# Optimization experiments

Hardware: AMD Instinct MI355X
Metric: run time of the kernel (lower is better)

## Reference

```python
import jax, jax.numpy as jnp
import numpy as np

D_MODEL = 768
EXPAND = 2
D_INNER = EXPAND * D_MODEL  # 1536
D_STATE = 16
D_CONV = 4
DT_RANK = D_MODEL // 16  # 48
N_LAYER = 3
BATCH, SEQLEN = 2, 1024
EPS = 1e-5


def setup_inputs() -> dict:
    key = jax.random.key(0)
    ks = jax.random.split(key, 8)
    s = 0.02
    hidden_states = jax.random.normal(ks[0], (BATCH, SEQLEN, D_MODEL), jnp.float32)
    norm_w = jnp.ones((N_LAYER, D_MODEL), jnp.float32)
    in_proj_w = s * jax.random.normal(ks[1], (N_LAYER, 2 * D_INNER, D_MODEL), jnp.float32)
    conv_w = s * jax.random.normal(ks[2], (N_LAYER, D_INNER, D_CONV), jnp.float32)
    conv_b = jnp.zeros((N_LAYER, D_INNER), jnp.float32)
    x_proj_w = s * jax.random.normal(ks[3], (N_LAYER, DT_RANK + 2 * D_STATE, D_INNER), jnp.float32)
    dt_proj_w = s * jax.random.normal(ks[4], (N_LAYER, D_INNER, DT_RANK), jnp.float32)
    dt_proj_b = jnp.full((N_LAYER, D_INNER), -4.6, jnp.float32)  # softplus ~ 0.01
    # S4D-real init: A_log = log(1..d_state), tiled over channels
    A_log = jnp.tile(jnp.log(jnp.arange(1, D_STATE + 1, dtype=jnp.float32))[None, None, :], (N_LAYER, D_INNER, 1))
    D_skip = jnp.ones((N_LAYER, D_INNER), jnp.float32)
    out_proj_w = s * jax.random.normal(ks[5], (N_LAYER, D_MODEL, D_INNER), jnp.float32)
    norm_f_w = jnp.ones((D_MODEL,), jnp.float32)
    return dict(hidden_states=hidden_states, norm_w=norm_w, in_proj_w=in_proj_w,
                conv_w=conv_w, conv_b=conv_b, x_proj_w=x_proj_w, dt_proj_w=dt_proj_w,
                dt_proj_b=dt_proj_b, A_log=A_log, D_skip=D_skip, out_proj_w=out_proj_w,
                norm_f_w=norm_f_w)


def _rmsnorm(x, w):
    return x * jax.lax.rsqrt(jnp.mean(x * x, axis=-1, keepdims=True) + EPS) * w


def _causal_conv1d(x, w, b):
    # x: [B, L, D]; w: [D, K] depthwise; left-pad for causality
    xt = jnp.transpose(x, (0, 2, 1))  # [B, D, L]
    y = jax.lax.conv_general_dilated(xt, w[:, None, :], window_strides=(1,),
                                     padding=[(D_CONV - 1, 0)], feature_group_count=D_INNER)
    return jnp.transpose(y, (0, 2, 1)) + b


def _selective_scan(u, delta, A, Bc, Cc, Dp):
    # u, delta: [B, L, D]; A: [D, N]; Bc, Cc: [B, L, N]
    def step(h, inp):
        dt, bt, ct, ut = inp  # [B,D], [B,N], [B,N], [B,D]
        h = jnp.exp(dt[..., None] * A) * h + (dt * ut)[..., None] * bt[:, None, :]
        y = jnp.einsum('bdn,bn->bd', h, ct)
        return h, y
    h0 = jnp.zeros((u.shape[0], u.shape[2], A.shape[1]), u.dtype)
    xs = (jnp.swapaxes(delta, 0, 1), jnp.swapaxes(Bc, 0, 1), jnp.swapaxes(Cc, 0, 1), jnp.swapaxes(u, 0, 1))
    _, ys = jax.lax.scan(step, h0, xs)  # ys: [L, B, D]
    return jnp.swapaxes(ys, 0, 1) + u * Dp


def _mixer(h, in_w, cw, cb, xw, dtw, dtb, A_log, Dp, ow):
    xz = jnp.einsum('bld,ed->ble', h, in_w)  # [B, L, 2*D_INNER]
    x, z = xz[..., :D_INNER], xz[..., D_INNER:]
    x = jax.nn.silu(_causal_conv1d(x, cw, cb))
    x_dbl = jnp.einsum('bld,ed->ble', x, xw)
    dt = x_dbl[..., :DT_RANK]
    Bc = x_dbl[..., DT_RANK:DT_RANK + D_STATE]
    Cc = x_dbl[..., DT_RANK + D_STATE:]
    delta = jax.nn.softplus(jnp.einsum('blr,dr->bld', dt, dtw) + dtb)
    A = -jnp.exp(A_log)
    y = _selective_scan(x, delta, A, Bc, Cc, Dp)
    y = y * jax.nn.silu(z)
    return jnp.einsum('bld,ed->ble', y, ow)


def reference(hidden_states, norm_w, in_proj_w, conv_w, conv_b, x_proj_w, dt_proj_w,
              dt_proj_b, A_log, D_skip, out_proj_w, norm_f_w):
    hidden = hidden_states
    residual = None
    for i in range(N_LAYER):
        residual = hidden if residual is None else hidden + residual  # fused add
        hidden = _rmsnorm(residual, norm_w[i])
        hidden = _mixer(hidden, in_proj_w[i], conv_w[i], conv_b[i], x_proj_w[i],
                        dt_proj_w[i], dt_proj_b[i], A_log[i], D_skip[i], out_proj_w[i])
    # final fused add + RMSNorm (prenorm=False)
    return _rmsnorm(hidden + residual, norm_f_w)
```

## Files before the change

### kernel.cpp

```cpp
#include <hip/hip_runtime.h>
#include <math.h>

#define D_MODEL 768
#define D_INNER 1536
#define D_STATE 16
#define D_CONV 4
#define DT_RANK 48
#define N_LAYER 3
#define BATCH 2
#define SEQLEN 1024
#define NROWS (BATCH * SEQLEN)
#define XDBL_W (DT_RANK + 2 * D_STATE)
#define EPS 1e-5f

#define SCHUNKS 64
#define SCLEN 16
#define SDN 16
#define KSPLIT 4
#define KSLICE (D_INNER / KSPLIT)

typedef short bf16x8 __attribute__((ext_vector_type(8)));
typedef float f32x4 __attribute__((ext_vector_type(4)));

__device__ __forceinline__ ushort f2bf(float x) {
    union { float f; uint u; } v; v.f = x;
    uint r = v.u + 0x7fff + ((v.u >> 16) & 1);
    return (ushort)(r >> 16);
}

__device__ __forceinline__ void gload_lds16(const void* g, void* l) {
    __builtin_amdgcn_global_load_lds(
        (const __attribute__((address_space(1))) unsigned int*)g,
        (__attribute__((address_space(3))) unsigned int*)l, 16, 0, 0);
}

__global__ __launch_bounds__(256) void cvt_bf16_kernel(
    const float* __restrict__ s, ushort* __restrict__ d, int n4)
{
    int i = blockIdx.x * 256 + threadIdx.x;
    if (i >= n4) return;
    float4 v = ((const float4*)s)[i];
    ushort4 o;
    o.x = f2bf(v.x); o.y = f2bf(v.y); o.z = f2bf(v.z); o.w = f2bf(v.w);
    ((ushort4*)d)[i] = o;
}

__global__ __launch_bounds__(256) void add_rmsnorm_kernel(
    const float* __restrict__ x, const float* __restrict__ res_in,
    const float* __restrict__ w, float* __restrict__ res_out,
    float* __restrict__ normed_f32, ushort* __restrict__ normed_bf)
{
    int row = blockIdx.x;
    int tid = threadIdx.x;
    const float* xr = x + row * D_MODEL;
    float v[3];
    float ss = 0.f;
#pragma unroll
    for (int i = 0; i < 3; i++) {
        int c = tid + i * 256;
        float t = xr[c];
        if (res_in) t += res_in[row * D_MODEL + c];
        v[i] = t;
        ss += t * t;
    }
    for (int off = 32; off; off >>= 1) ss += __shfl_xor(ss, off, 64);
    __shared__ float red[4];
    if ((tid & 63) == 0) red[tid >> 6] = ss;
    __syncthreads();
    float tot = red[0] + red[1] + red[2] + red[3];
    float scale = rsqrtf(tot * (1.f / D_MODEL) + EPS);
#pragma unroll
    for (int i = 0; i < 3; i++) {
        int c = tid + i * 256;
        if (res_out) res_out[row * D_MODEL + c] = v[i];
        float o = v[i] * scale * w[c];
        if (normed_f32) normed_f32[row * D_MODEL + c] = o;
        if (normed_bf)  normed_bf[row * D_MODEL + c] = f2bf(o);
    }
}

template <int BM, int BN>
__global__ __launch_bounds__(256) void gemm_mfma_kernel(
    const ushort* __restrict__ A, const ushort* __restrict__ W,
    float* __restrict__ C, int M, int N, int K)
{
    constexpr int TM = BM / 32;
    constexpr int TN = BN / 32;
    __shared__ __attribute__((aligned(16))) ushort As[BM * 64];
    __shared__ __attribute__((aligned(16))) ushort Ws[BN * 64];
    const int t = threadIdx.x;
    const int lane = t & 63, w = t >> 6;
    const int ln15 = lane & 15, q = lane >> 4;
    const int row0 = blockIdx.y * BM, col0 = blockIdx.x * BN;
    const int wm0 = (w & 1) * (BM / 2), wn0 = (w >> 1) * (BN / 2);

    f32x4 acc[TM][TN];
#pragma unroll
    for (int i = 0; i < TM; i++)
#pragma unroll
        for (int j = 0; j < TN; j++) acc[i][j] = (f32x4){0.f, 0.f, 0.f, 0.f};

    for (int k0 = 0; k0 < K; k0 += 64) {
        __syncthreads();
#pragma unroll
        for (int i = 0; i < BM / 32; i++) {
            int p = (i * 4 + w) * 64 + lane;
            int r = p >> 3, s = p & 7;
            int g = s ^ (r & 7);
            gload_lds16(A + (size_t)(row0 + r) * K + k0 + g * 8, &As[p * 8]);
        }
#pragma unroll
        for (int i = 0; i < BN / 32; i++) {
            int p = (i * 4 + w) * 64 + lane;
            int r = p >> 3, s = p & 7;
            int g = s ^ (r & 7);
            gload_lds16(W + (size_t)(col0 + r) * K + k0 + g * 8, &Ws[p * 8]);
        }
        __syncthreads();
#pragma unroll
        for (int ks = 0; ks < 2; ks++) {
            bf16x8 af[TM], wf[TN];
#pragma unroll
            for (int im = 0; im < TM; im++) {
                int m = wm0 + im * 16 + ln15;
                int slot = (ks * 4 + q) ^ (m & 7);
                af[im] = *(const bf16x8*)&As[m * 64 + slot * 8];
            }
#pragma unroll
            for (int jn = 0; jn < TN; jn++) {
                int n = wn0 + jn * 16 + ln15;
                int slot = (ks * 4 + q) ^ (n & 7);
                wf[jn] = *(const bf16x8*)&Ws[n * 64 + slot * 8];
            }
#pragma unroll
            for (int im = 0; im < TM; im++)
#pragma unroll
                for (int jn = 0; jn < TN; jn++)
                    acc[im][jn] = __builtin_amdgcn_mfma_f32_16x16x32_bf16(
                        af[im], wf[jn], acc[im][jn], 0, 0, 0);
        }
    }
#pragma unroll
    for (int im = 0; im < TM; im++) {
#pragma unroll
        for (int jn = 0; jn < TN; jn++) {
            int rr = row0 + wm0 + im * 16 + q * 4;
            int cc = col0 + wn0 + jn * 16 + ln15;
            float* cp = C + (size_t)rr * N + cc;
#pragma unroll
            for (int r = 0; r < 4; r++) cp[(size_t)r * N] = acc[im][jn][r];
        }
    }
}

template <int EPI>
__global__ __launch_bounds__(256) void gemm_kernel(
    const float* __restrict__ A, int lda,
    const float* __restrict__ W,
    const float* __restrict__ bias,
    float* __restrict__ C, int ldc,
    int M, int N, int K)
{
    __shared__ float As[16][64];
    __shared__ float Wsh[16][64];
    int tid = threadIdx.x;
    int row0 = blockIdx.y * 64;
    int col0 = blockIdx.x * 64;
    int lm = tid >> 2;
    int lk = (tid & 3) * 4;
    int ty = tid >> 4, tx = tid & 15;
    float acc[4][4] = {};
    const float* Arow = A + (size_t)(row0 + lm) * lda + lk;
    const float* Wrow = W + (size_t)(col0 + lm) * K + lk;
    bool wvalid = (col0 + lm) < N;

    for (int k0 = 0; k0 < K; k0 += 16) {
        float4 av = *(const float4*)(Arow + k0);
        float4 wv = wvalid ? *(const float4*)(Wrow + k0) : make_float4(0.f, 0.f, 0.f, 0.f);
        __syncthreads();
        As[lk + 0][lm] = av.x; As[lk + 1][lm] = av.y;
        As[lk + 2][lm] = av.z; As[lk + 3][lm] = av.w;
        Wsh[lk + 0][lm] = wv.x; Wsh[lk + 1][lm] = wv.y;
        Wsh[lk + 2][lm] = wv.z; Wsh[lk + 3][lm] = wv.w;
        __syncthreads();
#pragma unroll
        for (int k = 0; k < 16; k++) {
            float4 a = *(const float4*)&As[k][ty * 4];
            float4 b = *(const float4*)&Wsh[k][tx * 4];
            float ar[4] = {a.x, a.y, a.z, a.w};
            float br[4] = {b.x, b.y, b.z, b.w};
#pragma unroll
            for (int i = 0; i < 4; i++)
#pragma unroll
                for (int j = 0; j < 4; j++) acc[i][j] += ar[i] * br[j];
        }
    }
#pragma unroll
    for (int i = 0; i < 4; i++) {
        int r = row0 + ty * 4 + i;
#pragma unroll
        for (int j = 0; j < 4; j++) {
            int c = col0 + tx * 4 + j;
            if (c < N) {
                float v = acc[i][j];
                if (EPI == 1) {
                    v += bias[c];
                    v = (v > 20.f) ? v : log1pf(__expf(v));
                }
                C[(size_t)r * ldc + c] = v;
            }
        }
    }
}

__global__ __launch_bounds__(256) void gemm_xpart_kernel(
    const float* __restrict__ A, const float* __restrict__ W,
    float* __restrict__ Cp)
{
    __shared__ float As[16][64];
    __shared__ float Wsh[16][64];
    int tid = threadIdx.x;
    int row0 = blockIdx.y * 64;
    int col0 = blockIdx.x * 64;
    int kz = blockIdx.z * KSLICE;
    int lm = tid >> 2;
    int lk = (tid & 3) * 4;
    int ty = tid >> 4, tx = tid & 15;
    float acc[4][4] = {};
    const float* Arow = A + (size_t)(row0 + lm) * D_INNER + kz + lk;
    const float* Wrow = W + (size_t)(col0 + lm) * D_INNER + kz + lk;
    bool wvalid = (col0 + lm) < XDBL_W;

    for (int k0 = 0; k0 < KSLICE; k0 += 16) {
        float4 av = *(const float4*)(Arow + k0);
        float4 wv = wvalid ? *(const float4*)(Wrow + k0) : make_float4(0.f, 0.f, 0.f, 0.f);
        __syncthreads();
        As[lk + 0][lm] = av.x; As[lk + 1][lm] = av.y;
        As[lk + 2][lm] = av.z; As[lk + 3][lm] = av.w;
        Wsh[lk + 0][lm] = wv.x; Wsh[lk + 1][lm] = wv.y;
        Wsh[lk + 2][lm] = wv.z; Wsh[lk + 3][lm] = wv.w;
        __syncthreads();
#pragma unroll
        for (int k = 0; k < 16; k++) {
            float4 a = *(const float4*)&As[k][ty * 4];
            float4 b = *(const float4*)&Wsh[k][tx * 4];
            float ar[4] = {a.x, a.y, a.z, a.w};
            float br[4] = {b.x, b.y, b.z, b.w};
#pragma unroll
            for (int i = 0; i < 4; i++)
#pragma unroll
                for (int j = 0; j < 4; j++) acc[i][j] += ar[i] * br[j];
        }
    }
    float* Co = Cp + (size_t)blockIdx.z * NROWS * XDBL_W;
#pragma unroll
    for (int i = 0; i < 4; i++) {
        int r = row0 + ty * 4 + i;
#pragma unroll
        for (int j = 0; j < 4; j++) {
            int c = col0 + tx * 4 + j;
            if (c < XDBL_W) Co[(size_t)r * XDBL_W + c] = acc[i][j];
        }
    }
}

__global__ __launch_bounds__(256) void xreduce_kernel(
    const float* __restrict__ Cp, float* __restrict__ xdbl)
{
    int i = blockIdx.x * 256 + threadIdx.x;
    const int S4 = NROWS * XDBL_W / 4;
    if (i >= S4) return;
    const float4* p = (const float4*)Cp;
    float4 a = p[i], b = p[i + S4], c = p[i + 2 * S4], d = p[i + 3 * S4];
    float4 o;
    o.x = a.x + b.x + c.x + d.x;
    o.y = a.y + b.y + c.y + d.y;
    o.z = a.z + b.z + c.z + d.z;
    o.w = a.w + b.w + c.w + d.w;
    ((float4*)xdbl)[i] = o;
}

__global__ __launch_bounds__(256) void conv_silu_kernel(
    const float* __restrict__ xz, const float* __restrict__ cw,
    const float* __restrict__ cb, float* __restrict__ out)
{
    int idx = blockIdx.x * 256 + threadIdx.x;
    int d = idx % D_INNER;
    int bl = idx / D_INNER;
    int l = bl % SEQLEN;
    float s = cb[d];
    const float* xp = xz + (size_t)bl * (2 * D_INNER) + d;
#pragma unroll
    for (int k = 0; k < D_CONV; k++) {
        int ls = l - (D_CONV - 1) + k;
        if (ls >= 0) s += cw[d * D_CONV + k] * xp[(k - (D_CONV - 1)) * (2 * D_INNER)];
    }
    out[(size_t)bl * D_INNER + d] = s / (1.f + __expf(-s));
}

__global__ __launch_bounds__(1024) void scan2_kernel(
    const float* __restrict__ u, const float* __restrict__ delta,
    const float* __restrict__ A_log, const float* __restrict__ xdbl,
    const float* __restrict__ Dskip, const float* __restrict__ xz,
    ushort* __restrict__ ybf)
{
    __shared__ float PL[16][SDN * 17];
    __shared__ float HL[16][SDN * 17];
    const int t = threadIdx.x;
    const int lane = t & 63;
    const int w = t >> 6;
    const int dsub = lane & 15;
    const int csub = lane >> 4;
    const int c = w * 4 + csub;
    const int b = blockIdx.x / (D_INNER / SDN);
    const int d = (blockIdx.x % (D_INNER / SDN)) * SDN + dsub;

    float a2[D_STATE];
#pragma unroll
    for (int n = 0; n < D_STATE; n++)
        a2[n] = -__expf(A_log[d * D_STATE + n]) * 1.44269504f;

    const size_t base = (size_t)b * SEQLEN * D_INNER + d;
    const float* dtp = delta + base;
    const float* up  = u + base;
    const float* xrow = xdbl + (size_t)b * SEQLEN * XDBL_W;
    const int l0 = c * SCLEN;

    float h[D_STATE], P[D_STATE];
#pragma unroll
    for (int n = 0; n < D_STATE; n++) { h[n] = 0.f; P[n] = 1.f; }

    for (int i = 0; i < SCLEN; i++) {
        const int l = l0 + i;
        float dt = dtp[(size_t)l * D_INNER];
        float uu = up[(size_t)l * D_INNER];
        const float4* Bv = (const float4*)(xrow + (size_t)l * XDBL_W + DT_RANK);
        float4 q0 = Bv[0], q1 = Bv[1], q2 = Bv[2], q3 = Bv[3];
        float Bf[D_STATE] = {q0.x,q0.y,q0.z,q0.w, q1.x,q1.y,q1.z,q1.w,
                             q2.x,q2.y,q2.z,q2.w, q3.x,q3.y,q3.z,q3.w};
        float dtu = dt * uu;
#pragma unroll
        for (int n = 0; n < D_STATE; n++) {
            float e = __builtin_amdgcn_exp2f(dt * a2[n]);
            P[n] *= e;
            h[n] = e * h[n] + dtu * Bf[n];
        }
    }

#pragma unroll
    for (int n = 0; n < D_STATE; n++) {
        float Pp = __shfl(P[n], lane - 16, 64);
        float Hp = __shfl(h[n], lane - 16, 64);
        bool act = csub >= 1;
        h[n] = act ? P[n] * Hp + h[n] : h[n];
        P[n] = act ? P[n] * Pp : P[n];
    }
#pragma unroll
    for (int n = 0; n < D_STATE; n++) {
        float Pp = __shfl(P[n], lane - 32, 64);
        float Hp = __shfl(h[n], lane - 32, 64);
        bool act = csub >= 2;
        h[n] = act ? P[n] * Hp + h[n] : h[n];
        P[n] = act ? P[n] * Pp : P[n];
    }

    if (csub == 3) {
#pragma unroll
        for (int n = 0; n < D_STATE; n++) {
            PL[w][dsub * 17 + n] = P[n];
            HL[w][dsub * 17 + n] = h[n];
        }
    }
    __syncthreads();

    if (t < SDN * D_STATE) {
        const int d2 = t >> 4, n2 = t & 15;
        float hin = 0.f;
        for (int ww = 0; ww < 16; ww++) {
            float Pw = PL[ww][d2 * 17 + n2];
            float Hw = HL[ww][d2 * 17 + n2];
            HL[ww][d2 * 17 + n2] = hin;
            hin = Pw * hin + Hw;
        }
    }
    __syncthreads();

#pragma unroll
    for (int n = 0; n < D_STATE; n++) {
        float Win = HL[w][dsub * 17 + n];
        float Pe = __shfl(P[n], lane - 16, 64);
        float He = __shfl(h[n], lane - 16, 64);
        h[n] = (csub == 0) ? Win : Pe * Win + He;
    }

    const float Dsk = Dskip[d];
    const float* zp = xz + (size_t)b * SEQLEN * (2 * D_INNER) + D_INNER + d;
    ushort* yp = ybf + base;
    for (int i = 0; i < SCLEN; i++) {
        const int l = l0 + i;
        float dt = dtp[(size_t)l * D_INNER];
        float uu = up[(size_t)l * D_INNER];
        float zz = zp[(size_t)l * (2 * D_INNER)];
        const float4* Bv = (const float4*)(xrow + (size_t)l * XDBL_W + DT_RANK);
        float4 q0 = Bv[0], q1 = Bv[1], q2 = Bv[2], q3 = Bv[3];
        float4 r0 = Bv[4], r1 = Bv[5], r2 = Bv[6], r3 = Bv[7];
        float Bf[D_STATE] = {q0.x,q0.y,q0.z,q0.w, q1.x,q1.y,q1.z,q1.w,
                             q2.x,q2.y,q2.z,q2.w, q3.x,q3.y,q3.z,q3.w};
        float Cf[D_STATE] = {r0.x,r0.y,r0.z,r0.w, r1.x,r1.y,r1.z,r1.w,
                             r2.x,r2.y,r2.z,r2.w, r3.x,r3.y,r3.z,r3.w};
        float dtu = dt * uu;
        float acc = 0.f;
#pragma unroll
        for (int n = 0; n < D_STATE; n++) {
            float e = __builtin_amdgcn_exp2f(dt * a2[n]);
            h[n] = e * h[n] + dtu * Bf[n];
            acc += h[n] * Cf[n];
        }
        float yy = acc + uu * Dsk;
        float ee = __builtin_amdgcn_exp2f(-zz * 1.44269504f);
        float sil = zz * __builtin_amdgcn_rcpf(1.f + ee);
        yp[(size_t)l * D_INNER] = f2bf(yy * sil);
    }
}

extern "C" void kernel_launch(void* const* d_in, const int* in_sizes, int n_in,
                              void* d_out, int out_size, void* d_ws, size_t ws_size,
                              hipStream_t stream)
{
    const float* hs        = (const float*)d_in[0];
    const float* norm_w    = (const float*)d_in[1];
    const float* in_proj_w = (const float*)d_in[2];
    const float* conv_w    = (const float*)d_in[3];
    const float* conv_b    = (const float*)d_in[4];
    const float* x_proj_w  = (const float*)d_in[5];
    const float* dt_proj_w = (const float*)d_in[6];
    const float* dt_proj_b = (const float*)d_in[7];
    const float* A_log     = (const float*)d_in[8];
    const float* D_skip    = (const float*)d_in[9];
    const float* out_proj_w= (const float*)d_in[10];
    const float* norm_f_w  = (const float*)d_in[11];

    float* ws = (float*)d_ws;
    float* residual = ws;
    float* hidden   = residual + NROWS * D_MODEL;
    float* xz       = hidden + NROWS * D_MODEL;
    float* xconv    = xz + NROWS * 2 * D_INNER;
    float* xdbl     = xconv + NROWS * D_INNER;
    float* delta    = xdbl + NROWS * XDBL_W;
    float* xpart    = delta + NROWS * D_INNER;
    ushort* normbf  = (ushort*)(xpart + KSPLIT * NROWS * XDBL_W);
    ushort* ybf     = normbf + NROWS * D_MODEL;
    ushort* win_bf  = ybf + NROWS * D_INNER;
    ushort* wout_bf = win_bf + (size_t)N_LAYER * 2 * D_INNER * D_MODEL;

    {
        int n_in4  = N_LAYER * 2 * D_INNER * D_MODEL / 4;
        int n_out4 = N_LAYER * D_MODEL * D_INNER / 4;
        cvt_bf16_kernel<<<(n_in4 + 255) / 256, 256, 0, stream>>>(in_proj_w, win_bf, n_in4);
        cvt_bf16_kernel<<<(n_out4 + 255) / 256, 256, 0, stream>>>(out_proj_w, wout_bf, n_out4);
    }

    for (int i = 0; i < N_LAYER; i++) {
        add_rmsnorm_kernel<<<NROWS, 256, 0, stream>>>(
            i == 0 ? hs : hidden, i == 0 ? nullptr : residual,
            norm_w + i * D_MODEL, residual, nullptr, normbf);
        gemm_mfma_kernel<128, 128><<<dim3(2 * D_INNER / 128, NROWS / 128), 256, 0, stream>>>(
            normbf, win_bf + (size_t)i * 2 * D_INNER * D_MODEL,
            xz, NROWS, 2 * D_INNER, D_MODEL);
        conv_silu_kernel<<<NROWS * D_INNER / 256, 256, 0, stream>>>(
            xz, conv_w + i * D_INNER * D_CONV, conv_b + i * D_INNER, xconv);
        gemm_xpart_kernel<<<dim3(2, 32, KSPLIT), 256, 0, stream>>>(
            xconv, x_proj_w + (size_t)i * XDBL_W * D_INNER, xpart);
        xreduce_kernel<<<(NROWS * XDBL_W / 4 + 255) / 256, 256, 0, stream>>>(
            xpart, xdbl);
        gemm_kernel<1><<<dim3(24, 32), 256, 0, stream>>>(
            xdbl, XDBL_W, dt_proj_w + (size_t)i * D_INNER * DT_RANK,
            dt_proj_b + i * D_INNER, delta, D_INNER, NROWS, D_INNER, DT_RANK);
        scan2_kernel<<<BATCH * (D_INNER / SDN), 1024, 0, stream>>>(
            xconv, delta, A_log + (size_t)i * D_INNER * D_STATE, xdbl,
            D_skip + i * D_INNER, xz, ybf);
        gemm_mfma_kernel<128, 64><<<dim3(D_MODEL / 64, NROWS / 128), 256, 0, stream>>>(
            ybf, wout_bf + (size_t)i * D_MODEL * D_INNER,
            hidden, NROWS, D_MODEL, D_INNER);
    }
    add_rmsnorm_kernel<<<NROWS, 256, 0, stream>>>(
        hidden, residual, norm_f_w, nullptr, (float*)d_out, nullptr);
}
```

Baseline: 564.8 us.

## Move x_proj and dt_proj GEMMs onto bf16 MFMA and shrink GEMM tiles

Replaces the fp32 scalar GEMMs for x_proj (split-K) and dt_proj (softplus epilogue) with the bf16 MFMA GEMM. The new kernel gains a split-K mode, a bias/softplus epilogue and column bounds checking. Padded bf16 copies of x_proj and dt_proj weights are made once per call. conv_silu and xreduce now also write bf16 copies of their outputs to feed these GEMMs. The in_proj and out_proj GEMMs use smaller row tiles, which gives more blocks. The aim is to cut the FMA-bound fp32 GEMM time, at the cost of bf16 rounding in delta and x_dbl and extra conversion traffic.

```diff
diff --git a/kernel.cpp b/kernel.cpp
--- a/kernel.cpp
+++ b/kernel.cpp
@@ -13,11 +13,9 @@
 #define XDBL_W (DT_RANK + 2 * D_STATE)
 #define EPS 1e-5f
 
-#define SCHUNKS 64
 #define SCLEN 16
 #define SDN 16
-#define KSPLIT 4
-#define KSLICE (D_INNER / KSPLIT)
+#define KSPLIT_X 8
 
 typedef short bf16x8 __attribute__((ext_vector_type(8)));
 typedef float f32x4 __attribute__((ext_vector_type(4)));
@@ -45,6 +43,38 @@
     ((ushort4*)d)[i] = o;
 }
 
+__global__ __launch_bounds__(256) void cvt_xw_pad_kernel(
+    const float* __restrict__ src, ushort* __restrict__ dst)
+{
+    const int per = 128 * 1536 / 4;
+    int i = blockIdx.x * 256 + threadIdx.x;
+    if (i >= 3 * per) return;
+    int li = i / per, rem = i - li * per;
+    int r = (rem * 4) / 1536, c = (rem * 4) % 1536;
+    ushort4 o = make_ushort4(0, 0, 0, 0);
+    if (r < XDBL_W) {
+        const float* s = src + ((size_t)li * XDBL_W + r) * 1536 + c;
+        o.x = f2bf(s[0]); o.y = f2bf(s[1]); o.z = f2bf(s[2]); o.w = f2bf(s[3]);
+    }
+    ((ushort4*)dst)[i] = o;
+}
+
+__global__ __launch_bounds__(256) void cvt_dtw_pad_kernel(
+    const float* __restrict__ src, ushort* __restrict__ dst)
+{
+    const int per = 1536 * 64 / 4;
+    int i = blockIdx.x * 256 + threadIdx.x;
+    if (i >= 3 * per) return;
+    int li = i / per, rem = i - li * per;
+    int r = (rem * 4) / 64, c = (rem * 4) % 64;
+    ushort4 o = make_ushort4(0, 0, 0, 0);
+    if (c < DT_RANK) {
+        const float* s = src + ((size_t)li * 1536 + r) * DT_RANK + c;
+        o.x = f2bf(s[0]); o.y = f2bf(s[1]); o.z = f2bf(s[2]); o.w = f2bf(s[3]);
+    }
+    ((ushort4*)dst)[i] = o;
+}
+
 __global__ __launch_bounds__(256) void add_rmsnorm_kernel(
     const float* __restrict__ x, const float* __restrict__ res_in,
     const float* __restrict__ w, float* __restrict__ res_out,
@@ -79,10 +109,11 @@
     }
 }
 
-template <int BM, int BN>
+template <int BM, int BN, int EPI, int SPLITK>
 __global__ __launch_bounds__(256) void gemm_mfma_kernel(
     const ushort* __restrict__ A, const ushort* __restrict__ W,
-    float* __restrict__ C, int M, int N, int K)
+    const float* __restrict__ bias, float* __restrict__ C,
+    int ldc, int Nout, int M, int K)
 {
     constexpr int TM = BM / 32;
     constexpr int TN = BN / 32;
@@ -94,13 +125,17 @@
     const int row0 = blockIdx.y * BM, col0 = blockIdx.x * BN;
     const int wm0 = (w & 1) * (BM / 2), wn0 = (w >> 1) * (BN / 2);
 
+    int kper = K / SPLITK;
+    int kz = (SPLITK > 1) ? blockIdx.z * kper : 0;
+    if (SPLITK > 1) C += (size_t)blockIdx.z * M * ldc;
+
     f32x4 acc[TM][TN];
 #pragma unroll
     for (int i = 0; i < TM; i++)
 #pragma unroll
         for (int j = 0; j < TN; j++) acc[i][j] = (f32x4){0.f, 0.f, 0.f, 0.f};
 
-    for (int k0 = 0; k0 < K; k0 += 64) {
+    for (int k0 = kz; k0 < kz + kper; k0 += 64) {
         __syncthreads();
 #pragma unroll
         for (int i = 0; i < BM / 32; i++) {
@@ -146,143 +181,51 @@
         for (int jn = 0; jn < TN; jn++) {
             int rr = row0 + wm0 + im * 16 + q * 4;
             int cc = col0 + wn0 + jn * 16 + ln15;
-            float* cp = C + (size_t)rr * N + cc;
-#pragma unroll
-            for (int r = 0; r < 4; r++) cp[(size_t)r * N] = acc[im][jn][r];
-        }
-    }
-}
-
-template <int EPI>
-__global__ __launch_bounds__(256) void gemm_kernel(
-    const float* __restrict__ A, int lda,
-    const float* __restrict__ W,
-    const float* __restrict__ bias,
-    float* __restrict__ C, int ldc,
-    int M, int N, int K)
-{
-    __shared__ float As[16][64];
-    __shared__ float Wsh[16][64];
-    int tid = threadIdx.x;
-    int row0 = blockIdx.y * 64;
-    int col0 = blockIdx.x * 64;
-    int lm = tid >> 2;
-    int lk = (tid & 3) * 4;
-    int ty = tid >> 4, tx = tid & 15;
-    float acc[4][4] = {};
-    const float* Arow = A + (size_t)(row0 + lm) * lda + lk;
-    const float* Wrow = W + (size_t)(col0 + lm) * K + lk;
-    bool wvalid = (col0 + lm) < N;
-
-    for (int k0 = 0; k0 < K; k0 += 16) {
-        float4 av = *(const float4*)(Arow + k0);
-        float4 wv = wvalid ? *(const float4*)(Wrow + k0) : make_float4(0.f, 0.f, 0.f, 0.f);
-        __syncthreads();
-        As[lk + 0][lm] = av.x; As[lk + 1][lm] = av.y;
-        As[lk + 2][lm] = av.z; As[lk + 3][lm] = av.w;
-        Wsh[lk + 0][lm] = wv.x; Wsh[lk + 1][lm] = wv.y;
-        Wsh[lk + 2][lm] = wv.z; Wsh[lk + 3][lm] = wv.w;
-        __syncthreads();
-#pragma unroll
-        for (int k = 0; k < 16; k++) {
-            float4 a = *(const float4*)&As[k][ty * 4];
-            float4 b = *(const float4*)&Wsh[k][tx * 4];
-            float ar[4] = {a.x, a.y, a.z, a.w};
-            float br[4] = {b.x, b.y, b.z, b.w};
-#pragma unroll
-            for (int i = 0; i < 4; i++)
-#pragma unroll
-                for (int j = 0; j < 4; j++) acc[i][j] += ar[i] * br[j];
-        }
-    }
-#pragma unroll
-    for (int i = 0; i < 4; i++) {
-        int r = row0 + ty * 4 + i;
-#pragma unroll
-        for (int j = 0; j < 4; j++) {
-            int c = col0 + tx * 4 + j;
-            if (c < N) {
-                float v = acc[i][j];
-                if (EPI == 1) {
-                    v += bias[c];
-                    v = (v > 20.f) ? v : log1pf(__expf(v));
+            if (cc < Nout) {
+                float* cp = C + (size_t)rr * ldc + cc;
+#pragma unroll
+                for (int r = 0; r < 4; r++) {
+                    float v = acc[im][jn][r];
+                    if (EPI == 1) {
+                        v += bias[cc];
+                        v = (v > 20.f) ? v : log1pf(__expf(v));
+                    }
+                    cp[(size_t)r * ldc] = v;
                 }
-                C[(size_t)r * ldc + c] = v;
             }
         }
     }
 }
 
-__global__ __launch_bounds__(256) void gemm_xpart_kernel(
-    const float* __restrict__ A, const float* __restrict__ W,
-    float* __restrict__ Cp)
-{
-    __shared__ float As[16][64];
-    __shared__ float Wsh[16][64];
-    int tid = threadIdx.x;
-    int row0 = blockIdx.y * 64;
-    int col0 = blockIdx.x * 64;
-    int kz = blockIdx.z * KSLICE;
-    int lm = tid >> 2;
-    int lk = (tid & 3) * 4;
-    int ty = tid >> 4, tx = tid & 15;
-    float acc[4][4] = {};
-    const float* Arow = A + (size_t)(row0 + lm) * D_INNER + kz + lk;
-    const float* Wrow = W + (size_t)(col0 + lm) * D_INNER + kz + lk;
-    bool wvalid = (col0 + lm) < XDBL_W;
-
-    for (int k0 = 0; k0 < KSLICE; k0 += 16) {
-        float4 av = *(const float4*)(Arow + k0);
-        float4 wv = wvalid ? *(const float4*)(Wrow + k0) : make_float4(0.f, 0.f, 0.f, 0.f);
-        __syncthreads();
-        As[lk + 0][lm] = av.x; As[lk + 1][lm] = av.y;
-        As[lk + 2][lm] = av.z; As[lk + 3][lm] = av.w;
-        Wsh[lk + 0][lm] = wv.x; Wsh[lk + 1][lm] = wv.y;
-        Wsh[lk + 2][lm] = wv.z; Wsh[lk + 3][lm] = wv.w;
-        __syncthreads();
-#pragma unroll
-        for (int k = 0; k < 16; k++) {
-            float4 a = *(const float4*)&As[k][ty * 4];
-            float4 b = *(const float4*)&Wsh[k][tx * 4];
-            float ar[4] = {a.x, a.y, a.z, a.w};
-            float br[4] = {b.x, b.y, b.z, b.w};
-#pragma unroll
-            for (int i = 0; i < 4; i++)
-#pragma unroll
-                for (int j = 0; j < 4; j++) acc[i][j] += ar[i] * br[j];
-        }
-    }
-    float* Co = Cp + (size_t)blockIdx.z * NROWS * XDBL_W;
-#pragma unroll
-    for (int i = 0; i < 4; i++) {
-        int r = row0 + ty * 4 + i;
-#pragma unroll
-        for (int j = 0; j < 4; j++) {
-            int c = col0 + tx * 4 + j;
-            if (c < XDBL_W) Co[(size_t)r * XDBL_W + c] = acc[i][j];
-        }
-    }
-}
-
 __global__ __launch_bounds__(256) void xreduce_kernel(
-    const float* __restrict__ Cp, float* __restrict__ xdbl)
-{
+    const float* __restrict__ Cp, float* __restrict__ xdbl,
+    ushort* __restrict__ xdt)
+{
+    const int S4 = NROWS * XDBL_W / 4;
     int i = blockIdx.x * 256 + threadIdx.x;
-    const int S4 = NROWS * XDBL_W / 4;
     if (i >= S4) return;
     const float4* p = (const float4*)Cp;
-    float4 a = p[i], b = p[i + S4], c = p[i + 2 * S4], d = p[i + 3 * S4];
-    float4 o;
-    o.x = a.x + b.x + c.x + d.x;
-    o.y = a.y + b.y + c.y + d.y;
-    o.z = a.z + b.z + c.z + d.z;
-    o.w = a.w + b.w + c.w + d.w;
+    float4 o = p[i];
+#pragma unroll
+    for (int z = 1; z < KSPLIT_X; z++) {
+        float4 a = p[i + (size_t)z * S4];
+        o.x += a.x; o.y += a.y; o.z += a.z; o.w += a.w;
+    }
     ((float4*)xdbl)[i] = o;
+    int row = (i * 4) / XDBL_W, c0 = (i * 4) % XDBL_W;
+    if (c0 < DT_RANK) {
+        ushort4 b;
+        b.x = f2bf(o.x); b.y = f2bf(o.y); b.z = f2bf(o.z); b.w = f2bf(o.w);
+        *(ushort4*)&xdt[(size_t)row * 64 + c0] = b;
+    } else if (c0 < 64) {
+        *(ushort4*)&xdt[(size_t)row * 64 + c0] = make_ushort4(0, 0, 0, 0);
+    }
 }
 
 __global__ __launch_bounds__(256) void conv_silu_kernel(
     const float* __restrict__ xz, const float* __restrict__ cw,
-    const float* __restrict__ cb, float* __restrict__ out)
+    const float* __restrict__ cb, float* __restrict__ out,
+    ushort* __restrict__ out_bf)
 {
     int idx = blockIdx.x * 256 + threadIdx.x;
     int d = idx % D_INNER;
@@ -295,7 +238,9 @@
         int ls = l - (D_CONV - 1) + k;
         if (ls >= 0) s += cw[d * D_CONV + k] * xp[(k - (D_CONV - 1)) * (2 * D_INNER)];
     }
-    out[(size_t)bl * D_INNER + d] = s / (1.f + __expf(-s));
+    float sil = s / (1.f + __expf(-s));
+    out[(size_t)bl * D_INNER + d] = sil;
+    out_bf[(size_t)bl * D_INNER + d] = f2bf(sil);
 }
 
 __global__ __launch_bounds__(1024) void scan2_kernel(
@@ -448,40 +393,47 @@
     float* xdbl     = xconv + NROWS * D_INNER;
     float* delta    = xdbl + NROWS * XDBL_W;
     float* xpart    = delta + NROWS * D_INNER;
-    ushort* normbf  = (ushort*)(xpart + KSPLIT * NROWS * XDBL_W);
+    ushort* normbf  = (ushort*)(xpart + (size_t)KSPLIT_X * NROWS * XDBL_W);
     ushort* ybf     = normbf + NROWS * D_MODEL;
-    ushort* win_bf  = ybf + NROWS * D_INNER;
+    ushort* xconvbf = ybf + NROWS * D_INNER;
+    ushort* xdtbf   = xconvbf + NROWS * D_INNER;
+    ushort* win_bf  = xdtbf + NROWS * 64;
     ushort* wout_bf = win_bf + (size_t)N_LAYER * 2 * D_INNER * D_MODEL;
+    ushort* xw_pad  = wout_bf + (size_t)N_LAYER * D_MODEL * D_INNER;
+    ushort* dtw_pad = xw_pad + (size_t)N_LAYER * 128 * 1536;
 
     {
         int n_in4  = N_LAYER * 2 * D_INNER * D_MODEL / 4;
         int n_out4 = N_LAYER * D_MODEL * D_INNER / 4;
         cvt_bf16_kernel<<<(n_in4 + 255) / 256, 256, 0, stream>>>(in_proj_w, win_bf, n_in4);
         cvt_bf16_kernel<<<(n_out4 + 255) / 256, 256, 0, stream>>>(out_proj_w, wout_bf, n_out4);
+        cvt_xw_pad_kernel<<<(3 * 128 * 1536 / 4 + 255) / 256, 256, 0, stream>>>(x_proj_w, xw_pad);
+        cvt_dtw_pad_kernel<<<(3 * 1536 * 64 / 4 + 255) / 256, 256, 0, stream>>>(dt_proj_w, dtw_pad);
     }
 
     for (int i = 0; i < N_LAYER; i++) {
         add_rmsnorm_kernel<<<NROWS, 256, 0, stream>>>(
             i == 0 ? hs : hidden, i == 0 ? nullptr : residual,
             norm_w + i * D_MODEL, residual, nullptr, normbf);
-        gemm_mfma_kernel<128, 128><<<dim3(2 * D_INNER / 128, NROWS / 128), 256, 0, stream>>>(
-            normbf, win_bf + (size_t)i * 2 * D_INNER * D_MODEL,
-            xz, NROWS, 2 * D_INNER, D_MODEL);
+        gemm_mfma_kernel<64, 128, 0, 1><<<dim3(2 * D_INNER / 128, NROWS / 64), 256, 0, stream>>>(
+            normbf, win_bf + (size_t)i * 2 * D_INNER * D_MODEL, nullptr,
+            xz, 2 * D_INNER, 2 * D_INNER, NROWS, D_MODEL);
         conv_silu_kernel<<<NROWS * D_INNER / 256, 256, 0, stream>>>(
-            xz, conv_w + i * D_INNER * D_CONV, conv_b + i * D_INNER, xconv);
-        gemm_xpart_kernel<<<dim3(2, 32, KSPLIT), 256, 0, stream>>>(
-            xconv, x_proj_w + (size_t)i * XDBL_W * D_INNER, xpart);
+            xz, conv_w + i * D_INNER * D_CONV, conv_b + i * D_INNER, xconv, xconvbf);
+        gemm_mfma_kernel<64, 128, 0, KSPLIT_X><<<dim3(1, NROWS / 64, KSPLIT_X), 256, 0, stream>>>(
+            xconvbf, xw_pad + (size_t)i * 128 * 1536, nullptr,
+            xpart, XDBL_W, XDBL_W, NROWS, D_INNER);
         xreduce_kernel<<<(NROWS * XDBL_W / 4 + 255) / 256, 256, 0, stream>>>(
-            xpart, xdbl);
-        gemm_kernel<1><<<dim3(24, 32), 256, 0, stream>>>(
-            xdbl, XDBL_W, dt_proj_w + (size_t)i * D_INNER * DT_RANK,
-            dt_proj_b + i * D_INNER, delta, D_INNER, NROWS, D_INNER, DT_RANK);
+            xpart, xdbl, xdtbf);
+        gemm_mfma_kernel<128, 128, 1, 1><<<dim3(D_INNER / 128, NROWS / 128), 256, 0, stream>>>(
+            xdtbf, dtw_pad + (size_t)i * 1536 * 64, dt_proj_b + i * D_INNER,
+            delta, D_INNER, D_INNER, NROWS, 64);
         scan2_kernel<<<BATCH * (D_INNER / SDN), 1024, 0, stream>>>(
             xconv, delta, A_log + (size_t)i * D_INNER * D_STATE, xdbl,
             D_skip + i * D_INNER, xz, ybf);
-        gemm_mfma_kernel<128, 64><<<dim3(D_MODEL / 64, NROWS / 128), 256, 0, stream>>>(
-            ybf, wout_bf + (size_t)i * D_MODEL * D_INNER,
-            hidden, NROWS, D_MODEL, D_INNER);
+        gemm_mfma_kernel<64, 64, 0, 1><<<dim3(D_MODEL / 64, NROWS / 64), 256, 0, stream>>>(
+            ybf, wout_bf + (size_t)i * D_MODEL * D_INNER, nullptr,
+            hidden, D_MODEL, D_MODEL, NROWS, D_INNER);
     }
     add_rmsnorm_kernel<<<NROWS, 256, 0, stream>>>(
         hidden, residual, norm_f_w, nullptr, (float*)d_out, nullptr);
```

Measured after the change: 497.9 us. 1.13x faster.
